# Kernel optimization log

Measured on AMD Instinct MI355X. Metric: run time of the kernel, lower is better.

Reference implementation:

```python
import math
import jax, jax.numpy as jnp
import numpy as np

D_MODEL, D_HEAD, N_HEADS, COND = 1024, 64, 16, 1024
BATCH, L_T, H_S, W_S = 2, 8, 16, 16
N_FREQS = D_HEAD // 8  # rotary freqs per axis; 3 axes -> rotates 3*D_HEAD/4 dims
EPS = 1e-6


def _ste(x, qx):
    # straight-through estimator: forward qx, backward identity
    return x + jax.lax.stop_gradient(qx - x)


def _weight_quant(w):
    # BitNet-1.58 ternary: per-tensor absmean scale, round to {-1,0,1}
    s = 1.0 / jnp.clip(jnp.mean(jnp.abs(w)), 1e-5)
    return jnp.clip(jnp.round(w * s), -1.0, 1.0) / s


def _act_quant(x):
    # per-token int8 absmax quant
    s = 127.0 / jnp.clip(jnp.max(jnp.abs(x), axis=-1, keepdims=True), 1e-5)
    return jnp.clip(jnp.round(x * s), -128.0, 127.0) / s


def bit_linear(x, w):
    return _ste(x, _act_quant(x)) @ _ste(w, _weight_quant(w)).T


def rms_norm(x, scale, eps=EPS):
    ms = jnp.mean(x * x, axis=-1, keepdims=True)
    return x * scale * jax.lax.rsqrt(ms + eps)


def apply_rotary_emb(x, theta):
    # rotate first 2*d dims of x (d = theta.shape[-1]); pass the rest through
    d = theta.shape[-1]
    x1, x2, x3 = x[..., :d], x[..., d:2 * d], x[..., 2 * d:]
    cos, sin = jnp.cos(theta), jnp.sin(theta)
    return jnp.concatenate([x1 * cos - x2 * sin, x2 * cos + x1 * sin, x3], axis=-1)


def make_freqs():
    # log-spaced pi..10*pi, distributed across heads (k-diffusion AxialRoPE init)
    log_min, log_max = math.log(math.pi), math.log(10.0 * math.pi)
    f = jnp.exp(jnp.linspace(log_min, log_max, N_HEADS * N_FREQS + 1)[:-1])
    return f.reshape(N_FREQS, N_HEADS).T.astype(jnp.float32)  # [n_heads, n_freqs]


def setup_inputs() -> dict:
    key = jax.random.key(0)
    ks = jax.random.split(key, 6)
    x = jax.random.normal(ks[0], (BATCH, L_T, H_S, W_S, D_MODEL), jnp.float32)
    pos = jax.random.uniform(ks[1], (BATCH, L_T, H_S, W_S, 3), jnp.float32) * 2.0 - 1.0
    cond = jax.random.normal(ks[2], (BATCH, COND), jnp.float32)
    norm_w = jax.random.normal(ks[3], (D_MODEL, COND), jnp.float32) * 0.02
    qkv_w = jax.random.normal(ks[4], (3 * D_MODEL, D_MODEL), jnp.float32) * 0.02
    out_w = jax.random.normal(ks[5], (D_MODEL, D_MODEL), jnp.float32) * 0.02
    scale = jnp.full((N_HEADS,), 10.0, jnp.float32)
    freqs = make_freqs()
    return dict(x=x, pos=pos, cond=cond, norm_w=norm_w, qkv_w=qkv_w,
                out_w=out_w, scale=scale, freqs=freqs)


def reference(x, pos, cond, norm_w, qkv_w, out_w, scale, freqs):
    n, l, h, w, d = x.shape
    L = l * h * w
    skip = x
    # AdaRMSNorm: scale = 1 + zero-init Linear(cond)
    ada = 1.0 + cond @ norm_w.T                      # [n, d]
    xn = rms_norm(x, ada[:, None, None, None, :])
    # BitLinear QKV projection
    qkv = bit_linear(xn.reshape(n, L, d), qkv_w)     # [n, L, 3d]
    qkv = qkv.reshape(n, L, 3, N_HEADS, D_HEAD).transpose(2, 0, 3, 1, 4)  # [3,n,nh,L,e]
    q, k, v = qkv[0], qkv[1], qkv[2]
    # cosine-sim rescale with learned per-head scale
    sqrt_s = jnp.sqrt(scale)[:, None, None]          # [nh,1,1]
    q = q * (sqrt_s * jax.lax.rsqrt(jnp.sum(q * q, -1, keepdims=True) + EPS))
    k = k * (sqrt_s * jax.lax.rsqrt(jnp.sum(k * k, -1, keepdims=True) + EPS))
    # axial RoPE over 3 axes
    p = pos.reshape(n, L, 3)
    theta = jnp.concatenate([p[..., None, a:a + 1] * freqs for a in range(3)], axis=-1)  # [n,L,nh,3*nf]
    theta = jnp.moveaxis(theta, -2, -3)              # [n,nh,L,3*nf]
    q = apply_rotary_emb(q, theta)
    k = apply_rotary_emb(k, theta)
    # SDPA with scale=1.0 (cosine-sim already scaled)
    attn = jax.nn.softmax(jnp.einsum('nhqe,nhke->nhqk', q, k), axis=-1)
    o = jnp.einsum('nhqk,nhke->nhqe', attn, v)       # [n,nh,L,e]
    o = o.transpose(0, 2, 1, 3).reshape(n, L, d)
    o = bit_linear(o, out_w).reshape(n, l, h, w, d)
    return o + skip
```

## Files before the change

kernel.cpp:

```cpp
#include <hip/hip_runtime.h>
#include <hip/hip_bf16.h>
#include <math.h>

typedef __attribute__((ext_vector_type(8))) short bf16x8;
typedef __attribute__((ext_vector_type(4))) short bf16x4;
typedef __attribute__((ext_vector_type(4))) float f32x4;
typedef __attribute__((ext_vector_type(16))) float f32x16;
typedef __attribute__((ext_vector_type(4))) unsigned u32x4;
typedef __attribute__((ext_vector_type(2))) unsigned u32x2;
typedef __attribute__((ext_vector_type(4))) int i32x4;

#define DEV static __device__ __forceinline__
#define LOG2E 1.4426950408889634f

DEV unsigned short f2bf(float f) {
  unsigned int u = __float_as_uint(f);
  u += 0x7FFFu + ((u >> 16) & 1u);
  return (unsigned short)(u >> 16);
}
DEV float bf2f(unsigned short h) { return __uint_as_float(((unsigned int)h) << 16); }
DEV unsigned cvtpk(float lo, float hi) {
  unsigned r;
  asm("v_cvt_pk_bf16_f32 %0, %1, %2" : "=v"(r) : "v"(lo), "v"(hi));
  return r;
}
DEV float exp2raw(float x) {
  float r;
  asm("v_exp_f32 %0, %1" : "=v"(r) : "v"(x));
  return r;
}
DEV float wsum(float v) { for (int o = 32; o; o >>= 1) v += __shfl_xor(v, o); return v; }
DEV float wmaxr(float v) { for (int o = 32; o; o >>= 1) v = fmaxf(v, __shfl_xor(v, o)); return v; }

DEV void gload_lds16(const void* g, void* s) {
  __builtin_amdgcn_global_load_lds(
      (const __attribute__((address_space(1))) unsigned int*)g,
      (__attribute__((address_space(3))) unsigned int*)s, 16, 0, 0);
}

__global__ __launch_bounds__(256) void wred_k(const float* __restrict__ qw,
                                              const float* __restrict__ ow,
                                              float* __restrict__ rowsum) {
  int row = blockIdx.x;
  const float* p = (row < 3072) ? (qw + (size_t)row * 1024)
                                : (ow + (size_t)(row - 3072) * 1024);
  f32x4 v = *(const f32x4*)&p[threadIdx.x * 4];
  float s = fabsf(v[0]) + fabsf(v[1]) + fabsf(v[2]) + fabsf(v[3]);
  s = wsum(s);
  __shared__ float sh[4];
  if ((threadIdx.x & 63) == 0) sh[threadIdx.x >> 6] = s;
  __syncthreads();
  if (threadIdx.x == 0) rowsum[row] = sh[0] + sh[1] + sh[2] + sh[3];
}

__global__ __launch_bounds__(256) void finalize_k(const float* __restrict__ rowsum,
                                                  float* __restrict__ scales) {
  float s1 = 0.f, s2 = 0.f;
  for (int i = threadIdx.x; i < 3072; i += 256) s1 += rowsum[i];
  for (int i = threadIdx.x; i < 1024; i += 256) s2 += rowsum[3072 + i];
  s1 = wsum(s1); s2 = wsum(s2);
  __shared__ float sh1[4], sh2[4];
  if ((threadIdx.x & 63) == 0) { sh1[threadIdx.x >> 6] = s1; sh2[threadIdx.x >> 6] = s2; }
  __syncthreads();
  if (threadIdx.x == 0) {
    float m1 = fmaxf((sh1[0] + sh1[1] + sh1[2] + sh1[3]) / (3072.f * 1024.f), 1e-5f);
    float m2 = fmaxf((sh2[0] + sh2[1] + sh2[2] + sh2[3]) / (1024.f * 1024.f), 1e-5f);
    scales[0] = m1; scales[1] = 1.f / m1;
    scales[2] = m2; scales[3] = 1.f / m2;
  }
}

__global__ __launch_bounds__(256) void wquant_k(const float* __restrict__ qw,
                                                const float* __restrict__ ow,
                                                const float* __restrict__ scales,
                                                signed char* __restrict__ Wq,
                                                signed char* __restrict__ Wo) {
  int i0 = (blockIdx.x * 256 + threadIdx.x) * 4;
  if (i0 < 3072 * 1024) {
    f32x4 v = *(const f32x4*)&qw[i0];
    unsigned pk = 0;
    for (int j = 0; j < 4; j++) {
      int t = (int)fminf(fmaxf(rintf(v[j] * scales[1]), -1.f), 1.f);
      pk |= ((unsigned)t & 0xFFu) << (8 * j);
    }
    *(unsigned*)&Wq[i0] = pk;
  } else {
    int k = i0 - 3072 * 1024;
    f32x4 v = *(const f32x4*)&ow[k];
    unsigned pk = 0;
    for (int j = 0; j < 4; j++) {
      int t = (int)fminf(fmaxf(rintf(v[j] * scales[3]), -1.f), 1.f);
      pk |= ((unsigned)t & 0xFFu) << (8 * j);
    }
    *(unsigned*)&Wo[k] = pk;
  }
}

__global__ __launch_bounds__(256) void ada_k(const float* __restrict__ cond,
                                             const float* __restrict__ nw,
                                             float* __restrict__ ada) {
  int j = blockIdx.x * 4 + (threadIdx.x >> 6);
  int b = blockIdx.y;
  int l = threadIdx.x & 63;
  const float* cp = cond + b * 1024;
  const float* wp = nw + (size_t)j * 1024;
  float s = 0.f;
  for (int c = l; c < 1024; c += 64) s += cp[c] * wp[c];
  s = wsum(s);
  if (l == 0) ada[b * 1024 + j] = 1.f + s;
}

__global__ __launch_bounds__(256) void rmsq_k(const float* __restrict__ x,
                                              const float* __restrict__ ada,
                                              signed char* __restrict__ Aq,
                                              float* __restrict__ ascale) {
  int row = blockIdx.x;
  int b = row >> 11;
  const float* xr = x + (size_t)row * 1024;
  const float* ar = ada + b * 1024;
  int t4 = threadIdx.x * 4;
  f32x4 v = *(const f32x4*)&xr[t4];
  float ss = v[0]*v[0] + v[1]*v[1] + v[2]*v[2] + v[3]*v[3];
  ss = wsum(ss);
  __shared__ float sh[4], sh2[4];
  if ((threadIdx.x & 63) == 0) sh[threadIdx.x >> 6] = ss;
  __syncthreads();
  float inv = rsqrtf((sh[0] + sh[1] + sh[2] + sh[3]) * (1.f / 1024.f) + 1e-6f);
  f32x4 a = *(const f32x4*)&ar[t4];
  float xn[4]; float mx = 0.f;
  for (int i = 0; i < 4; i++) { xn[i] = v[i] * a[i] * inv; mx = fmaxf(mx, fabsf(xn[i])); }
  mx = wmaxr(mx);
  if ((threadIdx.x & 63) == 0) sh2[threadIdx.x >> 6] = mx;
  __syncthreads();
  float rmax = fmaxf(fmaxf(sh2[0], sh2[1]), fmaxf(sh2[2], sh2[3]));
  float s = 127.f / fmaxf(rmax, 1e-5f);
  unsigned pk = 0;
  for (int i = 0; i < 4; i++) {
    int ai = (int)fminf(fmaxf(rintf(xn[i] * s), -128.f), 127.f);
    pk |= ((unsigned)ai & 0xFFu) << (8 * i);
  }
  *(unsigned*)&Aq[(size_t)row * 1024 + t4] = pk;
  if (threadIdx.x == 0) ascale[row] = 1.f / s;
}

__global__ __launch_bounds__(256) void oquant_k(const unsigned short* __restrict__ Opart,
                                                const float* __restrict__ ms,
                                                signed char* __restrict__ Oq,
                                                float* __restrict__ oscale) {
  int row = blockIdx.x;
  int b = row >> 11, qrow = row & 2047;
  int t4 = threadIdx.x * 4;
  int h = t4 >> 6, e0 = t4 & 63;
  int bh = b * 16 + h;
  size_t i0 = (size_t)bh * 2048 + qrow;
  size_t i1 = (size_t)(32 + bh) * 2048 + qrow;
  float w = 1.f / (ms[i0] + ms[i1]);
  bf16x4 o0 = *(const bf16x4*)&Opart[i0 * 64 + e0];
  bf16x4 o1 = *(const bf16x4*)&Opart[i1 * 64 + e0];
  float v[4]; float mx = 0.f;
  for (int i = 0; i < 4; i++) {
    v[i] = (bf2f((unsigned short)o0[i]) + bf2f((unsigned short)o1[i])) * w;
    mx = fmaxf(mx, fabsf(v[i]));
  }
  mx = wmaxr(mx);
  __shared__ float sh[4];
  if ((threadIdx.x & 63) == 0) sh[threadIdx.x >> 6] = mx;
  __syncthreads();
  float rmax = fmaxf(fmaxf(sh[0], sh[1]), fmaxf(sh[2], sh[3]));
  float s = 127.f / fmaxf(rmax, 1e-5f);
  unsigned pk = 0;
  for (int i = 0; i < 4; i++) {
    int ai = (int)fminf(fmaxf(rintf(v[i] * s), -128.f), 127.f);
    pk |= ((unsigned)ai & 0xFFu) << (8 * i);
  }
  *(unsigned*)&Oq[(size_t)row * 1024 + t4] = pk;
  if (threadIdx.x == 0) oscale[row] = 1.f / s;
}

__global__ __launch_bounds__(256, 3) void gemm_i8(const signed char* __restrict__ A8,
                                                  const signed char* __restrict__ B8,
                                                  int N, int K, int nwg, int mode,
                                                  const float* __restrict__ rowsc,
                                                  const float* __restrict__ wscp,
                                                  const float* __restrict__ skip,
                                                  float* __restrict__ outF,
                                                  unsigned short* __restrict__ outB) {
  __shared__ signed char As[128 * 64];
  __shared__ signed char Bs[128 * 64];
  int bid = blockIdx.x;
  int wg = (bid % 8) * (nwg >> 3) + (bid >> 3);
  int bx = wg & 31, by = wg >> 5;
  int tid = threadIdx.x;
  int w = tid >> 6, l = tid & 63;
  int q = l & 15, g = l >> 4;
  int tm = bx * 128, tn = by * 128;
  int wr = w >> 1, wc = w & 1;
  float wsc = wscp[0];
  i32x4 acc[4][4];
  i32x4 zero = {0, 0, 0, 0};
#pragma unroll
  for (int m = 0; m < 4; m++)
#pragma unroll
    for (int n = 0; n < 4; n++) acc[m][n] = zero;
  int s0 = w * 64 + l, s1 = 256 + s0;
  int r0 = s0 >> 2, p0 = s0 & 3, gs0 = p0 ^ ((r0 >> 1) & 3);
  int r1 = s1 >> 2, p1 = s1 & 3, gs1 = p1 ^ ((r1 >> 1) & 3);
  const signed char* Ag0 = A8 + (size_t)(tm + r0) * K + gs0 * 16;
  const signed char* Ag1 = A8 + (size_t)(tm + r1) * K + gs1 * 16;
  const signed char* Bg0 = B8 + (size_t)(tn + r0) * K + gs0 * 16;
  const signed char* Bg1 = B8 + (size_t)(tn + r1) * K + gs1 * 16;
  int posq = ((q >> 1) & 3);
  for (int k0 = 0; k0 < K; k0 += 64) {
    gload_lds16(Ag0 + k0, &As[w * 1024]);
    gload_lds16(Ag1 + k0, &As[4096 + w * 1024]);
    gload_lds16(Bg0 + k0, &Bs[w * 1024]);
    gload_lds16(Bg1 + k0, &Bs[4096 + w * 1024]);
    __syncthreads();
    int pg = (g ^ posq) * 16;
    i32x4 af[4], bfr[4];
#pragma unroll
    for (int m = 0; m < 4; m++)
      af[m] = *(const i32x4*)&As[(wr * 64 + m * 16 + q) * 64 + pg];
#pragma unroll
    for (int n = 0; n < 4; n++)
      bfr[n] = *(const i32x4*)&Bs[(wc * 64 + n * 16 + q) * 64 + pg];
#pragma unroll
    for (int m = 0; m < 4; m++)
#pragma unroll
      for (int n = 0; n < 4; n++)
        acc[m][n] = __builtin_amdgcn_mfma_i32_16x16x64_i8(af[m], bfr[n], acc[m][n], 0, 0, 0);
    __syncthreads();
  }
#pragma unroll
  for (int m = 0; m < 4; m++) {
#pragma unroll
    for (int r = 0; r < 4; r++) {
      int row = tm + wr * 64 + m * 16 + g * 4 + r;
      float dq = rowsc[row] * wsc;
#pragma unroll
      for (int n = 0; n < 4; n++) {
        int col = tn + wc * 64 + n * 16 + q;
        float vv = (float)acc[m][n][r] * dq;
        if (mode == 0) outB[(size_t)row * N + col] = f2bf(vv);
        else { size_t idx = (size_t)row * N + col; outF[idx] = vv + skip[idx]; }
      }
    }
  }
}

__global__ __launch_bounds__(256) void prep_k(const unsigned short* __restrict__ qkv,
                                              const float* __restrict__ pos,
                                              const float* __restrict__ scale,
                                              const float* __restrict__ freqs,
                                              unsigned short* __restrict__ Qo,
                                              unsigned short* __restrict__ Ko,
                                              unsigned short* __restrict__ VT) {
  __shared__ unsigned short tile[64][72];
  int tid = threadIdx.x;
  if (blockIdx.x < 16384) {
    int w = tid >> 6, l = tid & 63;
    int gw = blockIdx.x * 4 + w;
    int h = gw & 15, t = (gw >> 4) & 2047, b = gw >> 15;
    const unsigned short* base = qkv + ((size_t)(b * 2048 + t)) * 3072 + h * 64 + l;
    float qv = bf2f(base[0]);
    float kv = bf2f(base[1024]);
    float sq = qv * qv, sk = kv * kv;
    for (int o = 32; o; o >>= 1) { sq += __shfl_xor(sq, o); sk += __shfl_xor(sk, o); }
    float ssc = sqrtf(scale[h]);
    float fq = ssc * rsqrtf(sq + 1e-6f);
    float fk = ssc * rsqrtf(sk + 1e-6f);
    float qn = qv * fq, kn = kv * fk;
    int e = l;
    int idx24 = (e < 24) ? e : e - 24;
    int partner = (e < 24) ? e + 24 : ((e < 48) ? e - 24 : e);
    float qo = __shfl(qn, partner), ko = __shfl(kn, partner);
    float qr = qn, kr = kn;
    if (e < 48) {
      int a = idx24 >> 3, f = idx24 & 7;
      float th = pos[((size_t)(b * 2048 + t)) * 3 + a] * freqs[h * 8 + f];
      float sn, cs; __sincosf(th, &sn, &cs);
      if (e < 24) { qr = qn * cs - qo * sn; kr = kn * cs - ko * sn; }
      else        { qr = qn * cs + qo * sn; kr = kn * cs + ko * sn; }
    }
    size_t oi = ((size_t)((b * 16 + h) * 2048 + t)) * 64 + e;
    Qo[oi] = f2bf(qr * LOG2E);
    Ko[oi] = f2bf(kr);
  } else {
    int bid2 = blockIdx.x - 16384;
    int tt = bid2 & 31, bh = bid2 >> 5;
    int b = bh >> 4, h = bh & 15;
    for (int ro = 0; ro < 2; ro++) {
      int r = ro * 32 + (tid >> 3);
      int c = (tid & 7) * 8;
      *(bf16x8*)&tile[r][c] =
          *(const bf16x8*)(qkv + ((size_t)(b * 2048 + tt * 64 + r)) * 3072 + 2048 + h * 64 + c);
    }
    __syncthreads();
    int e = tid >> 2;
    int tc = (tid & 3) * 16;
    bf16x8 o0, o1;
#pragma unroll
    for (int i = 0; i < 4; i++) {
      o0[i]     = (short)tile[tc + i][e];
      o0[4 + i] = (short)tile[tc + 8 + i][e];
      o1[i]     = (short)tile[tc + 4 + i][e];
      o1[4 + i] = (short)tile[tc + 12 + i][e];
    }
    unsigned short* dst = VT + ((size_t)(bh * 64 + e)) * 2048 + tt * 64 + tc;
    *(bf16x8*)dst = o0;
    *(bf16x8*)(dst + 8) = o1;
  }
}

__global__ __launch_bounds__(512, 4) void attn_k(const unsigned short* __restrict__ Q,
                                                 const unsigned short* __restrict__ K,
                                                 const unsigned short* __restrict__ VT,
                                                 unsigned short* __restrict__ Opart,
                                                 float* __restrict__ ms) {
  __shared__ unsigned short Ks[2][64 * 64];
  __shared__ unsigned short Vs[2][64 * 64];
  const float M0 = 15.0f;
  int tid = threadIdx.x;
  int w = tid >> 6, l = tid & 63;
  int q = l & 31, hi = l >> 5;
  int bx = blockIdx.x;
  int qg = bx & 7;
  int bh = (bx >> 3) & 31;
  int split = bx >> 8;
  int qrow0 = qg * 256 + w * 32;
  const unsigned short* Kbase = K + (size_t)bh * 2048 * 64 + (size_t)split * 1024 * 64;
  const unsigned short* Vbase = VT + (size_t)bh * 64 * 2048 + split * 1024;

  bf16x8 qa[4];
#pragma unroll
  for (int s = 0; s < 4; s++)
    qa[s] = *(const bf16x8*)(Q + ((size_t)bh * 2048 + qrow0 + q) * 64 + s * 16 + hi * 8);

  int off0[4], off1[4];
#pragma unroll
  for (int se = 0; se < 4; se++) {
    int gk = se * 2 + hi;
    off0[se] = q * 64 + ((gk ^ (q & 7)) * 8);
    off1[se] = (32 + q) * 64 + ((gk ^ (q & 7)) * 8);
  }

  int sl = w * 64 + l;
  int r0 = sl >> 3, g0 = (sl & 7) ^ (r0 & 7);
  const unsigned short* Kg0 = Kbase + (size_t)r0 * 64 + g0 * 8;
  const unsigned short* Vg0 = Vbase + (size_t)r0 * 2048 + g0 * 8;

  f32x16 acc0, acc1, fz;
  for (int i = 0; i < 16; i++) { acc0[i] = 0.f; acc1[i] = 0.f; fz[i] = 0.f; }
  float sum = 0.f;

  auto stage = [&](int buf, int kt) {
    gload_lds16(Kg0 + (size_t)kt * 64, &Ks[buf][w * 512]);
    gload_lds16(Vg0 + kt, &Vs[buf][w * 512]);
  };

  stage(0, 0);
  __syncthreads();
  int cur = 0;
  for (int it = 0; it < 16; it++) {
    if (it < 15) stage(cur ^ 1, (it + 1) * 64);
    const unsigned short* Ksc = Ks[cur];
    const unsigned short* Vsc = Vs[cur];

    bf16x8 ka0 = *(const bf16x8*)&Ksc[off0[0]];
    bf16x8 ka1 = *(const bf16x8*)&Ksc[off1[0]];
    __builtin_amdgcn_s_setprio(1);
    f32x16 s0 = __builtin_amdgcn_mfma_f32_32x32x16_bf16(ka0, qa[0], fz, 0, 0, 0);
    f32x16 s1 = __builtin_amdgcn_mfma_f32_32x32x16_bf16(ka1, qa[0], fz, 0, 0, 0);
#pragma unroll
    for (int se = 1; se < 4; se++) {
      ka0 = *(const bf16x8*)&Ksc[off0[se]];
      ka1 = *(const bf16x8*)&Ksc[off1[se]];
      s0 = __builtin_amdgcn_mfma_f32_32x32x16_bf16(ka0, qa[se], s0, 0, 0, 0);
      s1 = __builtin_amdgcn_mfma_f32_32x32x16_bf16(ka1, qa[se], s1, 0, 0, 0);
    }
    __builtin_amdgcn_s_setprio(0);

    bf16x8 pf[4];
#pragma unroll
    for (int n = 0; n < 4; n++) {
      int o = (n & 1) * 8;
      u32x4 t;
#pragma unroll
      for (int j = 0; j < 4; j++) {
        float a = (n < 2) ? s0[o + 2 * j] : s1[o + 2 * j];
        float b = (n < 2) ? s0[o + 2 * j + 1] : s1[o + 2 * j + 1];
        float e0 = exp2raw(a - M0);
        float e1 = exp2raw(b - M0);
        sum += e0 + e1;
        t[j] = cvtpk(e0, e1);
      }
      pf[n] = __builtin_bit_cast(bf16x8, t);
    }

    __builtin_amdgcn_s_setprio(1);
#pragma unroll
    for (int n = 0; n < 4; n++) {
      bf16x8 va0 = *(const bf16x8*)&Vsc[off0[n]];
      bf16x8 va1 = *(const bf16x8*)&Vsc[off1[n]];
      acc0 = __builtin_amdgcn_mfma_f32_32x32x16_bf16(va0, pf[n], acc0, 0, 0, 0);
      acc1 = __builtin_amdgcn_mfma_f32_32x32x16_bf16(va1, pf[n], acc1, 0, 0, 0);
    }
    __builtin_amdgcn_s_setprio(0);
    __syncthreads();
    cur ^= 1;
  }

  sum += __shfl_xor(sum, 32);
  size_t prow = (size_t)(split * 32 + bh) * 2048 + qrow0 + q;
  unsigned short* Op = Opart + prow * 64;
#pragma unroll
  for (int et = 0; et < 2; et++) {
    const f32x16& a = et ? acc1 : acc0;
#pragma unroll
    for (int qd = 0; qd < 4; qd++) {
      int e0 = et * 32 + 4 * hi + qd * 8;
      u32x2 t;
      t[0] = cvtpk(a[qd * 4 + 0], a[qd * 4 + 1]);
      t[1] = cvtpk(a[qd * 4 + 2], a[qd * 4 + 3]);
      *(bf16x4*)&Op[e0] = __builtin_bit_cast(bf16x4, t);
    }
  }
  if (hi == 0) ms[prow] = sum;
}

extern "C" void kernel_launch(void* const* d_in, const int* in_sizes, int n_in,
                              void* d_out, int out_size, void* d_ws, size_t ws_size,
                              hipStream_t stream) {
  const float* x      = (const float*)d_in[0];
  const float* pos    = (const float*)d_in[1];
  const float* cond   = (const float*)d_in[2];
  const float* norm_w = (const float*)d_in[3];
  const float* qkv_w  = (const float*)d_in[4];
  const float* out_w  = (const float*)d_in[5];
  const float* scale  = (const float*)d_in[6];
  const float* freqs  = (const float*)d_in[7];
  float* out = (float*)d_out;
  char* ws = (char*)d_ws;

  const size_t o_ada    = 0;
  const size_t o_rowsum = 8192;
  const size_t o_scales = 24576;
  const size_t o_ascale = 24832;
  const size_t o_oscale = 41216;
  const size_t o_Wq8    = 57600;
  const size_t o_Wo8    = o_Wq8 + 3145728;
  const size_t o_AqQ    = o_Wo8 + 1048576;
  const size_t o_qkv    = o_AqQ + 8388608;
  const size_t o_K      = o_qkv + 25165824;
  const size_t o_VT     = o_K + 8388608;

  float* ada            = (float*)(ws + o_ada);
  float* rowsum         = (float*)(ws + o_rowsum);
  float* scales         = (float*)(ws + o_scales);
  float* ascale         = (float*)(ws + o_ascale);
  float* oscale         = (float*)(ws + o_oscale);
  signed char* Wq8      = (signed char*)(ws + o_Wq8);
  signed char* Wo8      = (signed char*)(ws + o_Wo8);
  signed char* Aq8      = (signed char*)(ws + o_AqQ);
  unsigned short* Qb    = (unsigned short*)(ws + o_AqQ);
  unsigned short* qkv   = (unsigned short*)(ws + o_qkv);
  unsigned short* Opart = (unsigned short*)(ws + o_qkv);
  float* msb            = (float*)(ws + o_qkv + 2ull*32*2048*64*2);
  unsigned short* Kb    = (unsigned short*)(ws + o_K);
  signed char* Oq8      = (signed char*)(ws + o_K);
  unsigned short* VT    = (unsigned short*)(ws + o_VT);

  wred_k<<<4096, 256, 0, stream>>>(qkv_w, out_w, rowsum);
  finalize_k<<<1, 256, 0, stream>>>(rowsum, scales);
  wquant_k<<<4096, 256, 0, stream>>>(qkv_w, out_w, scales, Wq8, Wo8);
  ada_k<<<dim3(256, 2), 256, 0, stream>>>(cond, norm_w, ada);
  rmsq_k<<<4096, 256, 0, stream>>>(x, ada, Aq8, ascale);
  gemm_i8<<<768, 256, 0, stream>>>(Aq8, Wq8, 3072, 1024, 768, 0, ascale, &scales[0],
                                   nullptr, nullptr, qkv);
  prep_k<<<17408, 256, 0, stream>>>(qkv, pos, scale, freqs, Qb, Kb, VT);
  attn_k<<<512, 512, 0, stream>>>(Qb, Kb, VT, Opart, msb);
  oquant_k<<<4096, 256, 0, stream>>>(Opart, msb, Oq8, oscale);
  gemm_i8<<<256, 256, 0, stream>>>(Oq8, Wo8, 1024, 1024, 256, 1, oscale, &scales[2],
                                   x, out, nullptr);
}
```

Baseline: 154.0 us.

## Double attention KV tile per sync and remap block order for L2 locality

The attention kernel now stages 128 keys per iteration instead of 64. K and V^T are held in doubled LDS buffers and each iteration runs two 64-key sub-steps, which halves the number of barriers and loop iterations. Block indices are also remapped so that consecutive blocks share the same (split, head) across query groups, aiming to improve L2 reuse of K/V. The cost is twice the LDS footprint (64KB per block), which may lower occupancy relative to the launch bound of 4 blocks.

```diff
diff --git a/kernel.cpp b/kernel.cpp
--- a/kernel.cpp
+++ b/kernel.cpp
@@ -317,16 +317,16 @@
                                                  const unsigned short* __restrict__ VT,
                                                  unsigned short* __restrict__ Opart,
                                                  float* __restrict__ ms) {
-  __shared__ unsigned short Ks[2][64 * 64];
-  __shared__ unsigned short Vs[2][64 * 64];
+  __shared__ unsigned short Ks[2][128 * 64];
+  __shared__ unsigned short Vs[2][64 * 128];
   const float M0 = 15.0f;
   int tid = threadIdx.x;
   int w = tid >> 6, l = tid & 63;
   int q = l & 31, hi = l >> 5;
-  int bx = blockIdx.x;
-  int qg = bx & 7;
-  int bh = (bx >> 3) & 31;
-  int split = bx >> 8;
+  int bid = blockIdx.x;
+  int sbh = (bid >> 6) * 8 + (bid & 7);
+  int qg = (bid >> 3) & 7;
+  int split = sbh >> 5, bh = sbh & 31;
   int qrow0 = qg * 256 + w * 32;
   const unsigned short* Kbase = K + (size_t)bh * 2048 * 64 + (size_t)split * 1024 * 64;
   const unsigned short* Vbase = VT + (size_t)bh * 64 * 2048 + split * 1024;
@@ -336,76 +336,89 @@
   for (int s = 0; s < 4; s++)
     qa[s] = *(const bf16x8*)(Q + ((size_t)bh * 2048 + qrow0 + q) * 64 + s * 16 + hi * 8);
 
-  int off0[4], off1[4];
+  int koff0[4], koff1[4], voff0[4], voff1[4];
 #pragma unroll
   for (int se = 0; se < 4; se++) {
     int gk = se * 2 + hi;
-    off0[se] = q * 64 + ((gk ^ (q & 7)) * 8);
-    off1[se] = (32 + q) * 64 + ((gk ^ (q & 7)) * 8);
-  }
-
-  int sl = w * 64 + l;
-  int r0 = sl >> 3, g0 = (sl & 7) ^ (r0 & 7);
-  const unsigned short* Kg0 = Kbase + (size_t)r0 * 64 + g0 * 8;
-  const unsigned short* Vg0 = Vbase + (size_t)r0 * 2048 + g0 * 8;
+    koff0[se] = q * 64 + ((gk ^ (q & 7)) * 8);
+    koff1[se] = (32 + q) * 64 + ((gk ^ (q & 7)) * 8);
+    voff0[se] = q * 128 + ((gk ^ (q & 7)) * 8);
+    voff1[se] = (32 + q) * 128 + ((gk ^ (q & 7)) * 8);
+  }
+
+  int slA = tid, slB = 512 + tid;
+  int krA = slA >> 3, kgA = (slA & 7) ^ (krA & 7);
+  int krB = slB >> 3, kgB = (slB & 7) ^ (krB & 7);
+  int vrA = slA >> 4, vgA = (slA & 15) ^ (vrA & 7);
+  int vrB = slB >> 4, vgB = (slB & 15) ^ (vrB & 7);
+  const unsigned short* KgA = Kbase + (size_t)krA * 64 + kgA * 8;
+  const unsigned short* KgB = Kbase + (size_t)krB * 64 + kgB * 8;
+  const unsigned short* VgA = Vbase + (size_t)vrA * 2048 + vgA * 8;
+  const unsigned short* VgB = Vbase + (size_t)vrB * 2048 + vgB * 8;
 
   f32x16 acc0, acc1, fz;
   for (int i = 0; i < 16; i++) { acc0[i] = 0.f; acc1[i] = 0.f; fz[i] = 0.f; }
   float sum = 0.f;
 
   auto stage = [&](int buf, int kt) {
-    gload_lds16(Kg0 + (size_t)kt * 64, &Ks[buf][w * 512]);
-    gload_lds16(Vg0 + kt, &Vs[buf][w * 512]);
+    gload_lds16(KgA + (size_t)kt * 64, &Ks[buf][(w * 64) * 8]);
+    gload_lds16(KgB + (size_t)kt * 64, &Ks[buf][(512 + w * 64) * 8]);
+    gload_lds16(VgA + kt, &Vs[buf][(w * 64) * 8]);
+    gload_lds16(VgB + kt, &Vs[buf][(512 + w * 64) * 8]);
   };
 
   stage(0, 0);
   __syncthreads();
   int cur = 0;
-  for (int it = 0; it < 16; it++) {
-    if (it < 15) stage(cur ^ 1, (it + 1) * 64);
+  for (int it = 0; it < 8; it++) {
+    if (it < 7) stage(cur ^ 1, (it + 1) * 128);
     const unsigned short* Ksc = Ks[cur];
     const unsigned short* Vsc = Vs[cur];
-
-    bf16x8 ka0 = *(const bf16x8*)&Ksc[off0[0]];
-    bf16x8 ka1 = *(const bf16x8*)&Ksc[off1[0]];
-    __builtin_amdgcn_s_setprio(1);
-    f32x16 s0 = __builtin_amdgcn_mfma_f32_32x32x16_bf16(ka0, qa[0], fz, 0, 0, 0);
-    f32x16 s1 = __builtin_amdgcn_mfma_f32_32x32x16_bf16(ka1, qa[0], fz, 0, 0, 0);
-#pragma unroll
-    for (int se = 1; se < 4; se++) {
-      ka0 = *(const bf16x8*)&Ksc[off0[se]];
-      ka1 = *(const bf16x8*)&Ksc[off1[se]];
-      s0 = __builtin_amdgcn_mfma_f32_32x32x16_bf16(ka0, qa[se], s0, 0, 0, 0);
-      s1 = __builtin_amdgcn_mfma_f32_32x32x16_bf16(ka1, qa[se], s1, 0, 0, 0);
-    }
-    __builtin_amdgcn_s_setprio(0);
-
-    bf16x8 pf[4];
-#pragma unroll
-    for (int n = 0; n < 4; n++) {
-      int o = (n & 1) * 8;
-      u32x4 t;
-#pragma unroll
-      for (int j = 0; j < 4; j++) {
-        float a = (n < 2) ? s0[o + 2 * j] : s1[o + 2 * j];
-        float b = (n < 2) ? s0[o + 2 * j + 1] : s1[o + 2 * j + 1];
-        float e0 = exp2raw(a - M0);
-        float e1 = exp2raw(b - M0);
-        sum += e0 + e1;
-        t[j] = cvtpk(e0, e1);
+#pragma unroll
+    for (int ss = 0; ss < 2; ss++) {
+      int kro = ss * 4096;
+      int vco = ss * 64;
+      bf16x8 ka0 = *(const bf16x8*)&Ksc[kro + koff0[0]];
+      bf16x8 ka1 = *(const bf16x8*)&Ksc[kro + koff1[0]];
+      __builtin_amdgcn_s_setprio(1);
+      f32x16 s0 = __builtin_amdgcn_mfma_f32_32x32x16_bf16(ka0, qa[0], fz, 0, 0, 0);
+      f32x16 s1 = __builtin_amdgcn_mfma_f32_32x32x16_bf16(ka1, qa[0], fz, 0, 0, 0);
+#pragma unroll
+      for (int se = 1; se < 4; se++) {
+        ka0 = *(const bf16x8*)&Ksc[kro + koff0[se]];
+        ka1 = *(const bf16x8*)&Ksc[kro + koff1[se]];
+        s0 = __builtin_amdgcn_mfma_f32_32x32x16_bf16(ka0, qa[se], s0, 0, 0, 0);
+        s1 = __builtin_amdgcn_mfma_f32_32x32x16_bf16(ka1, qa[se], s1, 0, 0, 0);
       }
-      pf[n] = __builtin_bit_cast(bf16x8, t);
-    }
-
-    __builtin_amdgcn_s_setprio(1);
-#pragma unroll
-    for (int n = 0; n < 4; n++) {
-      bf16x8 va0 = *(const bf16x8*)&Vsc[off0[n]];
-      bf16x8 va1 = *(const bf16x8*)&Vsc[off1[n]];
-      acc0 = __builtin_amdgcn_mfma_f32_32x32x16_bf16(va0, pf[n], acc0, 0, 0, 0);
-      acc1 = __builtin_amdgcn_mfma_f32_32x32x16_bf16(va1, pf[n], acc1, 0, 0, 0);
-    }
-    __builtin_amdgcn_s_setprio(0);
+      __builtin_amdgcn_s_setprio(0);
+
+      bf16x8 pf[4];
+#pragma unroll
+      for (int n = 0; n < 4; n++) {
+        int o = (n & 1) * 8;
+        u32x4 t;
+#pragma unroll
+        for (int j = 0; j < 4; j++) {
+          float a = (n < 2) ? s0[o + 2 * j] : s1[o + 2 * j];
+          float b = (n < 2) ? s0[o + 2 * j + 1] : s1[o + 2 * j + 1];
+          float e0 = exp2raw(a - M0);
+          float e1 = exp2raw(b - M0);
+          sum += e0 + e1;
+          t[j] = cvtpk(e0, e1);
+        }
+        pf[n] = __builtin_bit_cast(bf16x8, t);
+      }
+
+      __builtin_amdgcn_s_setprio(1);
+#pragma unroll
+      for (int n = 0; n < 4; n++) {
+        bf16x8 va0 = *(const bf16x8*)&Vsc[vco + voff0[n]];
+        bf16x8 va1 = *(const bf16x8*)&Vsc[vco + voff1[n]];
+        acc0 = __builtin_amdgcn_mfma_f32_32x32x16_bf16(va0, pf[n], acc0, 0, 0, 0);
+        acc1 = __builtin_amdgcn_mfma_f32_32x32x16_bf16(va1, pf[n], acc1, 0, 0, 0);
+      }
+      __builtin_amdgcn_s_setprio(0);
+    }
     __syncthreads();
     cur ^= 1;
   }
```

After: 150.1 us. 2.5% less time.
